# Optimization experiments

Hardware: AMD Instinct MI355X
Metric: run time of the kernel (lower is better)

The kernel has to match this reference:

```python
import jax, jax.numpy as jnp
import numpy as np

K = 16  # top-k neighbors (init kwarg k)
EPS = 1e-8


def setup_inputs() -> dict:
    key = jax.random.key(0)
    # bs=8, closeness=12, flows=2, N=2048
    x_c = jax.random.normal(key, (8, 12, 2, 2048), dtype=jnp.float32)
    return {"x_c": x_c, "flow": 0}


def _cosine_adjacency(x):
    # x: (bs, 2, N, closeness) -> per-node feature = concat of both flows over time
    bs, f, N, c = x.shape
    feats = jnp.transpose(x, (0, 2, 1, 3)).reshape(bs, N, f * c)  # (bs, N, 2*closeness)
    fn = feats / (jnp.linalg.norm(feats, axis=-1, keepdims=True) + EPS)
    return jnp.einsum('bnd,bmd->bnm', fn, fn)  # (bs, N, N)


def reference(x_c, flow):
    # x_c: (bs, closeness, 2, N)
    bs, closeness, _, N = x_c.shape
    x = jnp.transpose(x_c, (0, 2, 3, 1)).astype(jnp.float32)  # (bs, 2, N, closeness)

    # mode == 'cos': cosine-similarity adjacency
    A = _cosine_adjacency(x)

    # index = argsort(A, descending)[:, :, :k]  ==  top-k neighbor indices per node
    _, index = jax.lax.top_k(A, K)  # (bs, N, K)

    # batched gather replacing the bs x N python double loop:
    # sx_c[i, j] = x[i, flow, index[i, j]]
    x_flow = x[:, flow]  # (bs, N, closeness)
    sx_c = jax.vmap(lambda xf, idx: xf[idx])(x_flow, index)  # (bs, N, K, closeness)

    # tgt_mode == 'c': tgt = x[:, flow].unsqueeze(-2)  -> (bs, N, 1, closeness)
    tgt = x_flow[:, :, None, :]
    # returned as tgt.permute(0,2,3,1).squeeze(1) -> (bs, closeness, N)
    tgt_out = jnp.squeeze(jnp.transpose(tgt, (0, 2, 3, 1)), axis=1)

    return sx_c, tgt_out
```

## Files before the change

### kernel.cpp

```cpp
#include <hip/hip_runtime.h>
#include <hip/hip_bf16.h>
#include <math.h>

#define BS   8
#define NPTS 2048
#define CCH  12
#define NF   2
#define DIM  24
#define KPAD 32
#define KTOP 16
#define NWV  8
#define RPB  16
#define CBUF 144
#define CBS  145

#define NROWS    (BS * NPTS)
#define TGT_BASE (NROWS * KTOP * CCH)

#define MARGIN 0.016f

typedef unsigned long long u64;
typedef unsigned int       u32;
typedef unsigned short     u16;
typedef __attribute__((ext_vector_type(8))) short short8;
typedef __attribute__((ext_vector_type(4))) float f32x4;

#define WS_FEATS 0
#define WS_RAW   (NROWS * DIM * 4)
#define WS_FHI   (WS_RAW + NROWS * CCH * 4)

__device__ __forceinline__ float np_norm_den(const float* __restrict__ v)
{
#pragma clang fp contract(off)
    float s[DIM];
    #pragma unroll
    for (int d = 0; d < DIM; ++d) s[d] = v[d] * v[d];
    float r[8];
    #pragma unroll
    for (int j = 0; j < 8; ++j) r[j] = (s[j] + s[j + 8]) + s[j + 16];
    float res = ((r[0] + r[1]) + (r[2] + r[3])) + ((r[4] + r[5]) + (r[6] + r[7]));
    return sqrtf(res) + 1e-8f;
}

__device__ __forceinline__ u32 ordf(float f)
{
    u32 u = __float_as_uint(f);
    return ((int)u >= 0) ? (u | 0x80000000u) : ~u;
}

__device__ __forceinline__ u16 bf16_rne(float x)
{
    u32 bits = __float_as_uint(x);
    bits += 0x7fffu + ((bits >> 16) & 1u);
    return (u16)(bits >> 16);
}

__device__ __forceinline__ void ins4(float& t0, float& t1, float& t2, float& t3, float v)
{
#if __has_builtin(__builtin_amdgcn_fmed3f)
    const float n0 = fmaxf(t0, v);
    const float n1 = __builtin_amdgcn_fmed3f(t0, t1, v);
    const float n2 = __builtin_amdgcn_fmed3f(t1, t2, v);
    const float n3 = __builtin_amdgcn_fmed3f(t2, t3, v);
#else
    const float n0 = fmaxf(t0, v);
    const float n1 = fmaxf(t1, fminf(t0, v));
    const float n2 = fmaxf(t2, fminf(t1, v));
    const float n3 = fmaxf(t3, fminf(t2, v));
#endif
    t0 = n0; t1 = n1; t2 = n2; t3 = n3;
}

#define CE(a, b) { const float h_ = fmaxf(a, b), l_ = fminf(a, b); a = h_; b = l_; }

__global__ __launch_bounds__(64) void prep_kernel(
    const float* __restrict__ x_c,
    const int*   __restrict__ flow_p,
    float*       __restrict__ feats,
    u16*         __restrict__ fhi,
    float*       __restrict__ raw,
    float*       __restrict__ out)
{
    const int t = blockIdx.x * 64 + threadIdx.x;
    const int b = t >> 11;
    const int n = t & (NPTS - 1);
    const float* xb = x_c + (size_t)b * CCH * NF * NPTS;

    float v[DIM];
    float fn[DIM];
    {
#pragma clang fp contract(off)
        #pragma unroll
        for (int c = 0; c < CCH; ++c)
            #pragma unroll
            for (int f = 0; f < NF; ++f)
                v[f * CCH + c] = xb[(c * NF + f) * NPTS + n];

        const float den = np_norm_den(v);
        #pragma unroll
        for (int d = 0; d < DIM; ++d) fn[d] = v[d] / den;
    }

    float* fo = feats + (size_t)t * DIM;
    #pragma unroll
    for (int j = 0; j < 6; ++j)
        *(f32x4*)(fo + 4 * j) = *(f32x4*)(fn + 4 * j);

    u16 hb[KPAD];
    #pragma unroll
    for (int d = 0; d < DIM; ++d) hb[d] = bf16_rne(fn[d]);
    #pragma unroll
    for (int d = DIM; d < KPAD; ++d) hb[d] = 0;

    u16* ho = fhi + (size_t)t * KPAD;
    #pragma unroll
    for (int j = 0; j < 4; ++j)
        *(short8*)(ho + 8 * j) = ((const short8*)hb)[j];

    const int flow = flow_p[0];
    float rv[CCH];
    #pragma unroll
    for (int c = 0; c < CCH; ++c) {
        rv[c] = flow ? v[CCH + c] : v[c];
        out[TGT_BASE + ((size_t)b * CCH + c) * NPTS + n] = rv[c];
    }
    float* ro = raw + (size_t)t * CCH;
    #pragma unroll
    for (int j = 0; j < 3; ++j)
        *(f32x4*)(ro + 4 * j) = *(f32x4*)(rv + 4 * j);
}

__global__ __launch_bounds__(512) void fused_topk_kernel(
    const float* __restrict__ feats,
    const u16*   __restrict__ fhi,
    const float* __restrict__ raw,
    float*       __restrict__ out)
{
    __shared__ union {
        f32x4 vk4[NWV * 16];
        u64   ckey[RPB * CBS];
    } sh;
    __shared__ float thr_s[RPB];
    __shared__ int   cnt[RPB];
    __shared__ int   sel[RPB][KTOP];

    const int tid  = threadIdx.x;
    const int lane = tid & 63;
    const int w    = __builtin_amdgcn_readfirstlane(tid >> 6);
    const int b     = blockIdx.x >> 7;
    const int chunk = blockIdx.x & 127;
    const int rb    = chunk * RPB;
    const int p     = lane & 15;
    const int q     = lane >> 4;

    if (tid < RPB) cnt[tid] = 0;

    short8 arow;
    {
        const size_t ae = ((size_t)(b * NPTS + rb + p)) * KPAD + q * 8;
        arow = *(const short8*)(fhi + ae);
    }

    float ta0 = -3.0f, ta1 = -3.0f, ta2 = -3.0f, ta3 = -3.0f;
    float tb0 = -3.0f, tb1 = -3.0f, tb2 = -3.0f, tb3 = -3.0f;
    {
        size_t be_n = ((size_t)(b * NPTS + w * 128 + p)) * KPAD + q * 8;
        short8 nb = *(const short8*)(fhi + be_n);
        #pragma unroll
        for (int t = 0; t < 8; ++t) {
            const short8 bh = nb;
            if (t < 7) {
                const size_t be = ((size_t)(b * NPTS + w * 128 + (t + 1) * 16 + p)) * KPAD + q * 8;
                nb = *(const short8*)(fhi + be);
            }
            f32x4 acc = {0.0f, 0.0f, 0.0f, 0.0f};
            acc = __builtin_amdgcn_mfma_f32_16x16x32_bf16(bh, arow, acc, 0, 0, 0);
            if (t & 1) {
                #pragma unroll
                for (int i = 0; i < 4; ++i) ins4(tb0, tb1, tb2, tb3, acc[i]);
            } else {
                #pragma unroll
                for (int i = 0; i < 4; ++i) ins4(ta0, ta1, ta2, ta3, acc[i]);
            }
        }
    }
    float t0 = fmaxf(ta0, tb3), t1 = fmaxf(ta1, tb2), t2 = fmaxf(ta2, tb1), t3 = fmaxf(ta3, tb0);
    CE(t0, t2) CE(t1, t3) CE(t0, t1) CE(t2, t3)

    #pragma unroll
    for (int x = 16; x <= 32; x <<= 1) {
        const float o0 = __shfl_xor(t0, x), o1 = __shfl_xor(t1, x);
        const float o2 = __shfl_xor(t2, x), o3 = __shfl_xor(t3, x);
        float m0 = fmaxf(t0, o3), m1 = fmaxf(t1, o2), m2 = fmaxf(t2, o1), m3 = fmaxf(t3, o0);
        CE(m0, m2) CE(m1, m3) CE(m0, m1) CE(m2, m3)
        t0 = m0; t1 = m1; t2 = m2; t3 = m3;
    }

    if (q == 0) {
        f32x4 v4 = {t0, t1, t2, t3};
        sh.vk4[w * 16 + p] = v4;
    }
    __syncthreads();

    if (w == 0) {
        const int j = q;
        const f32x4 A  = sh.vk4[j * 16 + p];
        const f32x4 Bv = sh.vk4[(j + 4) * 16 + p];
        float s0 = fmaxf(A[0], Bv[3]), s1 = fmaxf(A[1], Bv[2]);
        float s2 = fmaxf(A[2], Bv[1]), s3 = fmaxf(A[3], Bv[0]);
        float s4 = fminf(A[0], Bv[3]), s5 = fminf(A[1], Bv[2]);
        float s6 = fminf(A[2], Bv[1]), s7 = fminf(A[3], Bv[0]);
        CE(s0, s2) CE(s1, s3) CE(s0, s1) CE(s2, s3)
        CE(s4, s6) CE(s5, s7) CE(s4, s5) CE(s6, s7)
        float s[8] = {s0, s1, s2, s3, s4, s5, s6, s7};
        float t16[16];
        {
            float o[8];
            #pragma unroll
            for (int i = 0; i < 8; ++i) o[i] = __shfl_xor(s[i], 16);
            #pragma unroll
            for (int i = 0; i < 8; ++i) {
                t16[i]     = fmaxf(s[i], o[7 - i]);
                t16[8 + i] = fminf(s[i], o[7 - i]);
            }
            #pragma unroll
            for (int base = 0; base < 16; base += 8) {
                CE(t16[base + 0], t16[base + 4]) CE(t16[base + 1], t16[base + 5])
                CE(t16[base + 2], t16[base + 6]) CE(t16[base + 3], t16[base + 7])
                CE(t16[base + 0], t16[base + 2]) CE(t16[base + 1], t16[base + 3])
                CE(t16[base + 4], t16[base + 6]) CE(t16[base + 5], t16[base + 7])
                CE(t16[base + 0], t16[base + 1]) CE(t16[base + 2], t16[base + 3])
                CE(t16[base + 4], t16[base + 5]) CE(t16[base + 6], t16[base + 7])
            }
        }
        float z[16];
        #pragma unroll
        for (int i = 0; i < 16; ++i)
            z[i] = fmaxf(t16[i], __shfl_xor(t16[15 - i], 32));
        float mn = z[0];
        #pragma unroll
        for (int i = 1; i < 16; ++i) mn = fminf(mn, z[i]);
        if (q == 0) thr_s[p] = mn - MARGIN;
    }
    __syncthreads();

    const float thrp = thr_s[p];

    {
        size_t be_n = ((size_t)(b * NPTS + w * 256 + p)) * KPAD + q * 8;
        short8 nb = *(const short8*)(fhi + be_n);
        for (int t = 0; t < 16; ++t) {
            const int cb0 = w * 256 + t * 16;
            const short8 bh = nb;
            if (t < 15) {
                const size_t be = ((size_t)(b * NPTS + cb0 + 16 + p)) * KPAD + q * 8;
                nb = *(const short8*)(fhi + be);
            }
            f32x4 acc = {0.0f, 0.0f, 0.0f, 0.0f};
            acc = __builtin_amdgcn_mfma_f32_16x16x32_bf16(bh, arow, acc, 0, 0, 0);
            #pragma unroll
            for (int i = 0; i < 4; ++i) {
                if (acc[i] >= thrp) {
                    const int pos = atomicAdd(&cnt[p], 1);
                    if (pos < CBUF)
                        sh.ckey[p * CBS + pos] = (u64)(u32)(cb0 + q * 4 + i);
                }
            }
        }
    }
    __syncthreads();

    {
        const int r = tid & 15;
        const float* fr = feats + (size_t)(b * NPTS + rb + r) * DIM;
        float rfn[DIM];
        #pragma unroll
        for (int j = 0; j < 6; ++j)
            *(f32x4*)(rfn + 4 * j) = *(const f32x4*)(fr + 4 * j);
        const int e = (cnt[r] < CBUF) ? cnt[r] : CBUF;
        for (int pos = tid >> 4; pos < e; pos += 32) {
            const int idx = (int)(u32)sh.ckey[r * CBS + pos];
            const float* cp = feats + (size_t)(b * NPTS + idx) * DIM;
            float cv[DIM];
            #pragma unroll
            for (int j = 0; j < 6; ++j)
                *(f32x4*)(cv + 4 * j) = *(const f32x4*)(cp + 4 * j);
            float acc = 0.0f;
            #pragma unroll
            for (int d = 0; d < DIM; ++d)
                acc = __builtin_fmaf(cv[d], rfn[d], acc);
            sh.ckey[r * CBS + pos] = ((u64)ordf(acc) << 32) | (u32)(2047 - idx);
        }
    }
    __syncthreads();

    {
        const int L = tid >> 5;
        const int g = tid & 31;
        const int e = (cnt[L] < CBUF) ? cnt[L] : CBUF;
        const u64* rowbuf = &sh.ckey[L * CBS];
        for (int pos = g; pos < e; pos += 32) {
            const u64 key = rowbuf[pos];
            int rank = 0;
            for (int p2 = 0; p2 < e; ++p2) rank += (rowbuf[p2] > key);
            if (rank < KTOP) sel[L][rank] = 2047 - (int)(key & 0xFFFFFFFFull);
        }
    }
    __syncthreads();

    const int rg = b * NPTS + rb;
    for (int e2 = tid; e2 < RPB * KTOP * CCH; e2 += 512) {
        const int L = e2 / (KTOP * CCH);
        const int r = e2 % (KTOP * CCH);
        const int k = r / CCH;
        const int c = r % CCH;
        out[((size_t)(rg + L) * KTOP + k) * CCH + c] =
            raw[((size_t)b * NPTS + sel[L][k]) * CCH + c];
    }
}

extern "C" void kernel_launch(void* const* d_in, const int* in_sizes, int n_in,
                              void* d_out, int out_size, void* d_ws, size_t ws_size,
                              hipStream_t stream)
{
    const float* x_c    = (const float*)d_in[0];
    const int*   flow_p = (const int*)d_in[1];
    float*       out    = (float*)d_out;

    float* feats = (float*)((char*)d_ws + WS_FEATS);
    float* raw   = (float*)((char*)d_ws + WS_RAW);
    u16*   fhi   = (u16*)  ((char*)d_ws + WS_FHI);

    prep_kernel<<<NROWS / 64, 64, 0, stream>>>(x_c, flow_p, feats, fhi, raw, out);
    fused_topk_kernel<<<BS * 128, 512, 0, stream>>>(feats, fhi, raw, out);
}
```

Measured before the change: 93.34 us.

## Reuse first-pass MFMA scores packed as bf16 to skip half the candidate pass

The first pass, which sets the threshold, now covers columns 0-1023 and keeps its dot products packed as truncated 16-bit values in registers. The second pass filters those stored values instead of recomputing MFMAs, and only computes scores for columns 1024-2047. Every wave now computes the threshold redundantly, which removes one barrier and the shared threshold array. Loads use a three-deep prefetch and 32-bit index arithmetic. Because the stored scores are truncated, the margin and candidate buffer are enlarged so true neighbours are not missed, at the cost of more exact rescoring work and shared memory.

```diff
diff --git a/kernel.cpp b/kernel.cpp
--- a/kernel.cpp
+++ b/kernel.cpp
@@ -11,13 +11,13 @@
 #define KTOP 16
 #define NWV  8
 #define RPB  16
-#define CBUF 144
-#define CBS  145
+#define CBUF 176
+#define CBS  177
 
 #define NROWS    (BS * NPTS)
 #define TGT_BASE (NROWS * KTOP * CCH)
 
-#define MARGIN 0.016f
+#define MARGIN 0.024f
 
 typedef unsigned long long u64;
 typedef unsigned int       u32;
@@ -136,11 +136,8 @@
     const float* __restrict__ raw,
     float*       __restrict__ out)
 {
-    __shared__ union {
-        f32x4 vk4[NWV * 16];
-        u64   ckey[RPB * CBS];
-    } sh;
-    __shared__ float thr_s[RPB];
+    __shared__ f32x4 vk4[NWV * 16];
+    __shared__ u64   ckey[RPB * CBS];
     __shared__ int   cnt[RPB];
     __shared__ int   sel[RPB][KTOP];
 
@@ -157,24 +154,25 @@
 
     short8 arow;
     {
-        const size_t ae = ((size_t)(b * NPTS + rb + p)) * KPAD + q * 8;
+        const u32 ae = (u32)((b * NPTS + rb + p) * KPAD + q * 8);
         arow = *(const short8*)(fhi + ae);
     }
 
     float ta0 = -3.0f, ta1 = -3.0f, ta2 = -3.0f, ta3 = -3.0f;
     float tb0 = -3.0f, tb1 = -3.0f, tb2 = -3.0f, tb3 = -3.0f;
-    {
-        size_t be_n = ((size_t)(b * NPTS + w * 128 + p)) * KPAD + q * 8;
-        short8 nb = *(const short8*)(fhi + be_n);
+    u32 pkv[8][2];
+    {
+        const u32 base1 = (u32)((b * NPTS + w * 128 + p) * KPAD + q * 8);
+        short8 f0 = *(const short8*)(fhi + base1);
+        short8 f1 = *(const short8*)(fhi + base1 + 512);
+        short8 f2 = *(const short8*)(fhi + base1 + 1024);
         #pragma unroll
         for (int t = 0; t < 8; ++t) {
-            const short8 bh = nb;
-            if (t < 7) {
-                const size_t be = ((size_t)(b * NPTS + w * 128 + (t + 1) * 16 + p)) * KPAD + q * 8;
-                nb = *(const short8*)(fhi + be);
-            }
+            const short8 cur = f0;
+            f0 = f1; f1 = f2;
+            if (t + 3 < 8) f2 = *(const short8*)(fhi + base1 + (u32)(t + 3) * 512);
             f32x4 acc = {0.0f, 0.0f, 0.0f, 0.0f};
-            acc = __builtin_amdgcn_mfma_f32_16x16x32_bf16(bh, arow, acc, 0, 0, 0);
+            acc = __builtin_amdgcn_mfma_f32_16x16x32_bf16(cur, arow, acc, 0, 0, 0);
             if (t & 1) {
                 #pragma unroll
                 for (int i = 0; i < 4; ++i) ins4(tb0, tb1, tb2, tb3, acc[i]);
@@ -182,6 +180,10 @@
                 #pragma unroll
                 for (int i = 0; i < 4; ++i) ins4(ta0, ta1, ta2, ta3, acc[i]);
             }
+            pkv[t][0] = (__float_as_uint(acc[1]) & 0xffff0000u) |
+                        (__float_as_uint(acc[0]) >> 16);
+            pkv[t][1] = (__float_as_uint(acc[3]) & 0xffff0000u) |
+                        (__float_as_uint(acc[2]) >> 16);
         }
     }
     float t0 = fmaxf(ta0, tb3), t1 = fmaxf(ta1, tb2), t2 = fmaxf(ta2, tb1), t3 = fmaxf(ta3, tb0);
@@ -198,14 +200,15 @@
 
     if (q == 0) {
         f32x4 v4 = {t0, t1, t2, t3};
-        sh.vk4[w * 16 + p] = v4;
+        vk4[w * 16 + p] = v4;
     }
     __syncthreads();
 
-    if (w == 0) {
+    float thrp;
+    {
         const int j = q;
-        const f32x4 A  = sh.vk4[j * 16 + p];
-        const f32x4 Bv = sh.vk4[(j + 4) * 16 + p];
+        const f32x4 A  = vk4[j * 16 + p];
+        const f32x4 Bv = vk4[(j + 4) * 16 + p];
         float s0 = fmaxf(A[0], Bv[3]), s1 = fmaxf(A[1], Bv[2]);
         float s2 = fmaxf(A[2], Bv[1]), s3 = fmaxf(A[3], Bv[0]);
         float s4 = fminf(A[0], Bv[3]), s5 = fminf(A[1], Bv[2]);
@@ -240,47 +243,62 @@
         float mn = z[0];
         #pragma unroll
         for (int i = 1; i < 16; ++i) mn = fminf(mn, z[i]);
-        if (q == 0) thr_s[p] = mn - MARGIN;
+        thrp = mn - MARGIN;
+    }
+
+    const u32 base2 = (u32)((b * NPTS + 1024 + w * 128 + p) * KPAD + q * 8);
+    short8 g0 = *(const short8*)(fhi + base2);
+    short8 g1 = *(const short8*)(fhi + base2 + 512);
+    short8 g2 = *(const short8*)(fhi + base2 + 1024);
+
+    #pragma unroll
+    for (int t = 0; t < 8; ++t) {
+        const int cb0 = w * 128 + t * 16 + q * 4;
+        #pragma unroll
+        for (int h = 0; h < 2; ++h) {
+            const u32 r = pkv[t][h];
+            const float v0 = __uint_as_float(r << 16);
+            const float v1 = __uint_as_float(r & 0xffff0000u);
+            if (v0 >= thrp) {
+                const int pos = atomicAdd(&cnt[p], 1);
+                if (pos < CBUF) ckey[p * CBS + pos] = (u64)(u32)(cb0 + 2 * h);
+            }
+            if (v1 >= thrp) {
+                const int pos = atomicAdd(&cnt[p], 1);
+                if (pos < CBUF) ckey[p * CBS + pos] = (u64)(u32)(cb0 + 2 * h + 1);
+            }
+        }
+    }
+
+    #pragma unroll
+    for (int t = 0; t < 8; ++t) {
+        const short8 cur = g0;
+        g0 = g1; g1 = g2;
+        if (t + 3 < 8) g2 = *(const short8*)(fhi + base2 + (u32)(t + 3) * 512);
+        f32x4 acc = {0.0f, 0.0f, 0.0f, 0.0f};
+        acc = __builtin_amdgcn_mfma_f32_16x16x32_bf16(cur, arow, acc, 0, 0, 0);
+        const int cb0 = 1024 + w * 128 + t * 16 + q * 4;
+        #pragma unroll
+        for (int i = 0; i < 4; ++i) {
+            if (acc[i] >= thrp) {
+                const int pos = atomicAdd(&cnt[p], 1);
+                if (pos < CBUF) ckey[p * CBS + pos] = (u64)(u32)(cb0 + i);
+            }
+        }
     }
     __syncthreads();
 
-    const float thrp = thr_s[p];
-
-    {
-        size_t be_n = ((size_t)(b * NPTS + w * 256 + p)) * KPAD + q * 8;
-        short8 nb = *(const short8*)(fhi + be_n);
-        for (int t = 0; t < 16; ++t) {
-            const int cb0 = w * 256 + t * 16;
-            const short8 bh = nb;
-            if (t < 15) {
-                const size_t be = ((size_t)(b * NPTS + cb0 + 16 + p)) * KPAD + q * 8;
-                nb = *(const short8*)(fhi + be);
-            }
-            f32x4 acc = {0.0f, 0.0f, 0.0f, 0.0f};
-            acc = __builtin_amdgcn_mfma_f32_16x16x32_bf16(bh, arow, acc, 0, 0, 0);
-            #pragma unroll
-            for (int i = 0; i < 4; ++i) {
-                if (acc[i] >= thrp) {
-                    const int pos = atomicAdd(&cnt[p], 1);
-                    if (pos < CBUF)
-                        sh.ckey[p * CBS + pos] = (u64)(u32)(cb0 + q * 4 + i);
-                }
-            }
-        }
-    }
-    __syncthreads();
-
     {
         const int r = tid & 15;
-        const float* fr = feats + (size_t)(b * NPTS + rb + r) * DIM;
+        const float* fr = feats + (u32)((b * NPTS + rb + r) * DIM);
         float rfn[DIM];
         #pragma unroll
         for (int j = 0; j < 6; ++j)
             *(f32x4*)(rfn + 4 * j) = *(const f32x4*)(fr + 4 * j);
         const int e = (cnt[r] < CBUF) ? cnt[r] : CBUF;
         for (int pos = tid >> 4; pos < e; pos += 32) {
-            const int idx = (int)(u32)sh.ckey[r * CBS + pos];
-            const float* cp = feats + (size_t)(b * NPTS + idx) * DIM;
+            const int idx = (int)(u32)ckey[r * CBS + pos];
+            const float* cp = feats + (u32)((b * NPTS + idx) * DIM);
             float cv[DIM];
             #pragma unroll
             for (int j = 0; j < 6; ++j)
@@ -289,7 +307,7 @@
             #pragma unroll
             for (int d = 0; d < DIM; ++d)
                 acc = __builtin_fmaf(cv[d], rfn[d], acc);
-            sh.ckey[r * CBS + pos] = ((u64)ordf(acc) << 32) | (u32)(2047 - idx);
+            ckey[r * CBS + pos] = ((u64)ordf(acc) << 32) | (u32)(2047 - idx);
         }
     }
     __syncthreads();
@@ -298,7 +316,7 @@
         const int L = tid >> 5;
         const int g = tid & 31;
         const int e = (cnt[L] < CBUF) ? cnt[L] : CBUF;
-        const u64* rowbuf = &sh.ckey[L * CBS];
+        const u64* rowbuf = &ckey[L * CBS];
         for (int pos = g; pos < e; pos += 32) {
             const u64 key = rowbuf[pos];
             int rank = 0;
@@ -315,7 +333,7 @@
         const int k = r / CCH;
         const int c = r % CCH;
         out[((size_t)(rg + L) * KTOP + k) * CCH + c] =
-            raw[((size_t)b * NPTS + sel[L][k]) * CCH + c];
+            raw[(u32)((b * NPTS + sel[L][k]) * CCH) + c];
     }
 }
 
```

Result: slower. 97.64 us (+4.6%).
